# Performance work log

Measured on AMD Instinct MI355X. Metric: run time of the kernel, lower is better.

Reference implementation:

```python
import jax, jax.numpy as jnp
import numpy as np

N, H, MSG, OUT = 512, 128, 128, 64
F1, F2 = 256, 256  # f_dims (also used for g_mlp per source)
GOUT = 128         # hardcoded output_gmlp_dim
O1 = 256           # o_dims


def _p(key, shape, scale):
    return jax.random.normal(key, shape, dtype=jnp.float32) * scale


def setup_inputs() -> dict:
    key = jax.random.key(0)
    ks = jax.random.split(key, 24)
    s = lambda fan_in: 1.0 / np.sqrt(fan_in)
    inp = {
        "x": jax.random.normal(ks[0], (N, H), dtype=jnp.float32),
        "hidden": jax.random.normal(ks[1], (N, H), dtype=jnp.float32),
        "h0": jnp.zeros((1, N, H), dtype=jnp.float32),
        "c0": jnp.zeros((1, N, H), dtype=jnp.float32),
        # f MLP: 2H -> F1 -> F2 -> MSG
        "Wf1": _p(ks[2], (F1, 2 * H), s(2 * H)), "bf1": jnp.zeros((F1,), jnp.float32),
        "Wf2": _p(ks[3], (F2, F1), s(F1)), "bf2": jnp.zeros((F2,), jnp.float32),
        "Wf3": _p(ks[4], (MSG, F2), s(F2)), "bf3": jnp.zeros((MSG,), jnp.float32),
        # g_mlp: H+MSG -> F1 -> F2 -> GOUT
        "Wg1": _p(ks[5], (F1, H + MSG), s(H + MSG)), "bg1": jnp.zeros((F1,), jnp.float32),
        "Wg2": _p(ks[6], (F2, F1), s(F1)), "bg2": jnp.zeros((F2,), jnp.float32),
        "Wg3": _p(ks[7], (GOUT, F2), s(F2)), "bg3": jnp.zeros((GOUT,), jnp.float32),
        # LSTM (1 layer): GOUT -> H, gate order i,f,g,o
        "W_ih": _p(ks[8], (4 * H, GOUT), s(H)), "W_hh": _p(ks[9], (4 * H, H), s(H)),
        "b_ih": jnp.zeros((4 * H,), jnp.float32), "b_hh": jnp.zeros((4 * H,), jnp.float32),
        # o MLP: H -> O1 -> OUT
        "Wo1": _p(ks[10], (O1, H), s(H)), "bo1": jnp.zeros((O1,), jnp.float32),
        "Wo2": _p(ks[11], (OUT, O1), s(O1)), "bo2": jnp.zeros((OUT,), jnp.float32),
    }
    return inp


def reference(x, hidden, h0, c0,
              Wf1, bf1, Wf2, bf2, Wf3, bf3,
              Wg1, bg1, Wg2, bg2, Wg3, bg3,
              W_ih, W_hh, b_ih, b_hh,
              Wo1, bo1, Wo2, bo2):
    # --- pairwise message MLP f(cat(hidden[i], hidden[j])) over all (i,j) ---
    # split first-layer weight to avoid materializing [N,N,2H] concat
    A = hidden @ Wf1[:, :H].T            # [N, F1], contribution of node i
    B = hidden @ Wf1[:, H:].T            # [N, F1], contribution of node j
    h1 = jax.nn.relu(A[:, None, :] + B[None, :, :] + bf1)   # [N, N, F1]
    h2 = jax.nn.relu(h1 @ Wf2.T + bf2)                       # [N, N, F2]
    messages = h2 @ Wf3.T + bf3                              # [N, N, MSG]
    sum_messages = jnp.sum(messages, axis=0)                 # [N, MSG] (sum over i)

    # --- g_mlp on cat(x, sum_messages) ---
    g_in = jnp.concatenate([x, sum_messages], axis=1)        # [N, H+MSG]
    g1 = jax.nn.relu(g_in @ Wg1.T + bg1)
    g2 = jax.nn.relu(g1 @ Wg2.T + bg2)
    input_g = g2 @ Wg3.T + bg3                               # [N, GOUT]

    # --- single-step LSTM (seq_len=1, batch=N), PyTorch gate order i,f,g,o ---
    gates = input_g @ W_ih.T + b_ih + h0[0] @ W_hh.T + b_hh  # [N, 4H]
    i_g, f_g, g_g, o_g = jnp.split(gates, 4, axis=1)
    i_g = jax.nn.sigmoid(i_g); f_g = jax.nn.sigmoid(f_g)
    g_g = jnp.tanh(g_g); o_g = jax.nn.sigmoid(o_g)
    c_new = f_g * c0[0] + i_g * g_g
    hidden_new = o_g * jnp.tanh(c_new)                       # [N, H]

    # --- output MLP o (single_output=False) ---
    o1 = jax.nn.relu(hidden_new @ Wo1.T + bo1)
    out = o1 @ Wo2.T + bo2                                   # [N, OUT]

    return (out, hidden_new, hidden_new[None], c_new[None])
```

## Files before the change

### kernel.cpp

```cpp
#include <hip/hip_runtime.h>
#include <hip/hip_bf16.h>


#define NN   512
#define HH   128
#define F1D  256
#define F2D  256
#define OUTD 64
#define ICHUNK 64

typedef _Float16 half_t;
typedef _Float16 half8 __attribute__((ext_vector_type(8)));
typedef float float4_t __attribute__((ext_vector_type(4)));
typedef float float8_t __attribute__((ext_vector_type(8)));

__device__ __forceinline__ float sigmoidf_(float x) {
    return 1.0f / (1.0f + __expf(-x));
}

#define HL_INV 2.44140625e-4f

#define WS_TAIL_B 1835008
#define WS_WT1_B  3342336
#define T3H 0
#define G1H 65536
#define G2H 196608
#define G3H 327680
#define CATH 393216
#define O1H 655360
#define O2H 720896

__constant__ int p_cum[8]   = {16, 24, 40, 56, 64, 96, 112, 116};
__constant__ int p_K[8]     = {256, 256, 256, 256, 256, 256, 128, 256};
__constant__ int p_hioff[8] = {0, T3H, G1H, G2H, G3H, CATH, O1H, O2H};
__constant__ int p_cnt[8]   = {65536, 32768, 65536, 65536, 32768, 131072, 32768, 16384};

__global__ __launch_bounds__(256)
void k0_prep(const float* __restrict__ Wf1,
             const float* __restrict__ Wf2,
             const float* __restrict__ Wf3,
             const float* __restrict__ Wg1, const float* __restrict__ Wg2,
             const float* __restrict__ Wg3,
             const float* __restrict__ W_ih, const float* __restrict__ W_hh,
             const float* __restrict__ Wo1, const float* __restrict__ Wo2,
             half_t* __restrict__ tail,
             half_t* __restrict__ W2H, half_t* __restrict__ W2L,
             float* __restrict__ WT1) {
    __shared__ float slab[4096];
    __shared__ float tile[64][65];
    const int t = threadIdx.x;
    const int bid = blockIdx.x;

    if (bid < 116) {
        int m = 0;
        while (m < 7 && bid >= p_cum[m]) ++m;
        const int pl = bid - (m ? p_cum[m - 1] : 0);
        const int K = p_K[m];
        const int kshift = (K == 256) ? 8 : 7;
        const int n0 = pl * 16;

        const float* src;
        switch (m) {
            case 0: src = Wf2; break;
            case 1: src = Wf3; break;
            case 2: src = Wg1; break;
            case 3: src = Wg2; break;
            case 4: src = Wg3; break;
            case 6: src = Wo1; break;
            default: src = Wo2; break;
        }
        for (int q = t; q < (16 * K) / 4; q += 256) {
            const int flat = q * 4;
            const int r = flat >> kshift;
            const int k = flat & (K - 1);
            float4_t v;
            if (m == 5) {
                v = (k < 128) ? *(const float4_t*)(W_ih + (n0 + r) * 128 + k)
                              : *(const float4_t*)(W_hh + (n0 + r) * 128 + (k - 128));
            } else {
                v = *(const float4_t*)(src + (size_t)(n0 + r) * K + k);
            }
            *(float4_t*)&slab[flat] = v;
        }
        __syncthreads();

        half_t *hi, *lo;
        if (m == 0) { hi = W2H; lo = W2L; }
        else        { hi = tail + p_hioff[m]; lo = hi + p_cnt[m]; }
        const int base = pl * (K << 4);
        for (int f0 = t * 8; f0 < 16 * K; f0 += 2048) {
            const int ks = f0 >> 9;
            const int g4 = (f0 >> 7) & 3;
            const int l15 = (f0 >> 3) & 15;
            const int k0 = ks * 32 + g4 * 8;
            float8_t v = *(const float8_t*)&slab[l15 * K + k0];
            half8 hv, lv;
#pragma unroll
            for (int e = 0; e < 8; ++e) {
                half_t h = (half_t)v[e];
                hv[e] = h;
                lv[e] = (half_t)((v[e] - (float)h) * 4096.0f);
            }
            *(half8*)(hi + base + f0) = hv;
            *(half8*)(lo + base + f0) = lv;
        }
    } else {
        const int local = bid - 116;
        const int tr = local >> 2, tc = local & 3;
#pragma unroll
        for (int q = 0; q < 16; ++q) {
            const int idx = q * 256 + t;
            const int ly = idx >> 6, lx = idx & 63;
            tile[ly][lx] = Wf1[(tr * 64 + ly) * 256 + tc * 64 + lx];
        }
        __syncthreads();
#pragma unroll
        for (int q = 0; q < 16; ++q) {
            const int idx = q * 256 + t;
            const int ly = idx >> 6, lx = idx & 63;
            WT1[(tc * 64 + ly) * 256 + tr * 64 + lx] = tile[lx][ly];
        }
    }
}

__global__ __launch_bounds__(256)
void k1_proj(const float* __restrict__ hidden,
             const float* __restrict__ WT1,
             const float* __restrict__ bf1,
             float* __restrict__ A32,
             float* __restrict__ B32) {
    __shared__ float hid[4][HH];
    const int t = threadIdx.x;
    const int i0 = blockIdx.x * 4;
    for (int q = t; q < 4 * HH; q += 256)
        hid[q >> 7][q & 127] = hidden[(i0 + (q >> 7)) * HH + (q & 127)];
    __syncthreads();

    float accA[4], accB[4];
    const float b = bf1[t];
#pragma unroll
    for (int r = 0; r < 4; ++r) { accA[r] = b; accB[r] = 0.0f; }

    const float* wcol = WT1 + t;
#pragma unroll 4
    for (int kk = 0; kk < HH; ++kk) {
        const float va = wcol[kk * 256];
        const float vb = wcol[(kk + 128) * 256];
#pragma unroll
        for (int r = 0; r < 4; ++r) {
            const float h = hid[r][kk];
            accA[r] = fmaf(h, va, accA[r]);
            accB[r] = fmaf(h, vb, accB[r]);
        }
    }
#pragma unroll
    for (int r = 0; r < 4; ++r) {
        A32[(i0 + r) * F1D + t] = accA[r];
        B32[(i0 + r) * F1D + t] = accB[r];
    }
}

__global__ __launch_bounds__(512, 2)
void k2_pairwise(const float* __restrict__ A32,
                 const float* __restrict__ B32,
                 const half_t* __restrict__ W2H,
                 const half_t* __restrict__ W2L,
                 const float* __restrict__ bf2,
                 float* __restrict__ S) {
    __shared__ half_t hbuf[2][8][512];

    const int tid = threadIdx.x;
    const int lane = tid & 63;
    const int w = tid >> 6;
    const int l15 = lane & 15;
    const int g4 = lane >> 4;
    const int j0 = blockIdx.y * 16;
    const int i0 = blockIdx.x * ICHUNK;

    const half8* WH8 = (const half8*)W2H;
    const half8* WL8 = (const half8*)W2L;
    half8 Wh[2][8], Wl[2][8];
#pragma unroll
    for (int nt = 0; nt < 2; ++nt)
#pragma unroll
        for (int ks = 0; ks < 8; ++ks) {
            const int idx = (w * 2 + nt) * 512 + ks * 64 + lane;
            Wh[nt][ks] = WH8[idx];
            Wl[nt][ks] = WL8[idx];
        }
#pragma unroll
    for (int nt = 0; nt < 2; ++nt)
#pragma unroll
        for (int ks = 0; ks < 8; ++ks) {
            asm volatile("" : "+v"(Wh[nt][ks]));
            asm volatile("" : "+v"(Wl[nt][ks]));
        }

    float4_t Bw0 = *(const float4_t*)(B32 + (size_t)(j0 + l15) * F1D + w * 32 + g4 * 8);
    float4_t Bw1 = *(const float4_t*)(B32 + (size_t)(j0 + l15) * F1D + w * 32 + g4 * 8 + 4);
    asm volatile("" : "+v"(Bw0));
    asm volatile("" : "+v"(Bw1));

    float b2v[2];
#pragma unroll
    for (int nt = 0; nt < 2; ++nt) b2v[nt] = bf2[w * 32 + nt * 16 + l15];

    float4_t acc[2];
#pragma unroll
    for (int nt = 0; nt < 2; ++nt)
#pragma unroll
        for (int r = 0; r < 4; ++r) acc[nt][r] = 0.0f;

    {
        const float* Ap = A32 + (size_t)i0 * F1D + w * 32 + g4 * 8;
        float4_t a0 = *(const float4_t*)Ap;
        float4_t a1 = *(const float4_t*)(Ap + 4);
        half8 hf;
#pragma unroll
        for (int e = 0; e < 4; ++e) {
            hf[e]     = (half_t)fmaxf(a0[e] + Bw0[e], 0.0f);
            hf[4 + e] = (half_t)fmaxf(a1[e] + Bw1[e], 0.0f);
        }
        *(half8*)&hbuf[0][w][lane * 8] = hf;
    }
    __syncthreads();

    int p = 0;
    for (int io = 0; io < ICHUNK; ++io) {
        float4_t a0, a1;
        if (io + 1 < ICHUNK) {
            const float* Ap = A32 + (size_t)(i0 + io + 1) * F1D + w * 32 + g4 * 8;
            a0 = *(const float4_t*)Ap;
            a1 = *(const float4_t*)(Ap + 4);
        }

        float4_t C[2], Cl[2];
#pragma unroll
        for (int nt = 0; nt < 2; ++nt)
#pragma unroll
            for (int r = 0; r < 4; ++r) { C[nt][r] = 0.0f; Cl[nt][r] = 0.0f; }

#pragma unroll
        for (int ks = 0; ks < 8; ++ks) {
            half8 hf = *(const half8*)&hbuf[p][ks][lane * 8];
            C[0]  = __builtin_amdgcn_mfma_f32_16x16x32_f16(hf, Wh[0][ks], C[0], 0, 0, 0);
            C[1]  = __builtin_amdgcn_mfma_f32_16x16x32_f16(hf, Wh[1][ks], C[1], 0, 0, 0);
            Cl[0] = __builtin_amdgcn_mfma_f32_16x16x32_f16(hf, Wl[0][ks], Cl[0], 0, 0, 0);
            Cl[1] = __builtin_amdgcn_mfma_f32_16x16x32_f16(hf, Wl[1][ks], Cl[1], 0, 0, 0);
        }

        if (io + 1 < ICHUNK) {
            half8 hf;
#pragma unroll
            for (int e = 0; e < 4; ++e) {
                hf[e]     = (half_t)fmaxf(a0[e] + Bw0[e], 0.0f);
                hf[4 + e] = (half_t)fmaxf(a1[e] + Bw1[e], 0.0f);
            }
            *(half8*)&hbuf[p ^ 1][w][lane * 8] = hf;
        }

#pragma unroll
        for (int nt = 0; nt < 2; ++nt) {
#pragma unroll
            for (int r = 0; r < 4; ++r) {
                float v = fmaf(Cl[nt][r], HL_INV, C[nt][r]) + b2v[nt];
                acc[nt][r] += fmaxf(v, 0.0f);
            }
        }
        __syncthreads();
        p ^= 1;
    }

#pragma unroll
    for (int nt = 0; nt < 2; ++nt)
#pragma unroll
        for (int r = 0; r < 4; ++r)
            atomicAdd(&S[(size_t)(j0 + g4 * 4 + r) * F2D + w * 32 + nt * 16 + l15], acc[nt][r]);
}

#define AST 260

template<int NT, int NKS>
__device__ __forceinline__ void frag_gemm(const float* __restrict__ aPtr,
                                          const half_t* __restrict__ WhF,
                                          const half_t* __restrict__ WlF,
                                          const int* pB, int lane8,
                                          float4_t* Chi, float4_t* Clo) {
#pragma unroll
    for (int ks = 0; ks < NKS; ++ks) {
        float4_t a0 = *(const float4_t*)(aPtr + ks * 32);
        float4_t a1 = *(const float4_t*)(aPtr + ks * 32 + 4);
        half8 ah, al;
#pragma unroll
        for (int e = 0; e < 4; ++e) {
            half_t h0 = (half_t)a0[e];
            ah[e] = h0; al[e] = (half_t)((a0[e] - (float)h0) * 4096.0f);
            half_t h1 = (half_t)a1[e];
            ah[4+e] = h1; al[4+e] = (half_t)((a1[e] - (float)h1) * 4096.0f);
        }
#pragma unroll
        for (int nt = 0; nt < NT; ++nt) {
            half8 wh = *(const half8*)(WhF + pB[nt] + ks * 512 + lane8);
            half8 wl = *(const half8*)(WlF + pB[nt] + ks * 512 + lane8);
            Chi[nt] = __builtin_amdgcn_mfma_f32_16x16x32_f16(ah, wh, Chi[nt], 0, 0, 0);
            Clo[nt] = __builtin_amdgcn_mfma_f32_16x16x32_f16(ah, wl, Clo[nt], 0, 0, 0);
            Clo[nt] = __builtin_amdgcn_mfma_f32_16x16x32_f16(al, wh, Clo[nt], 0, 0, 0);
        }
    }
}

__global__ __launch_bounds__(512)
void k4_tail(const float* __restrict__ S,
             const float* __restrict__ x,
             const float* __restrict__ h0,
             const float* __restrict__ c0,
             const half_t* __restrict__ tail,
             const float* __restrict__ bf3,
             const float* __restrict__ bg1, const float* __restrict__ bg2,
             const float* __restrict__ bg3,
             const float* __restrict__ b_ih, const float* __restrict__ b_hh,
             const float* __restrict__ bo1, const float* __restrict__ bo2,
             float* __restrict__ out,
             float* __restrict__ hid_out,
             float* __restrict__ h_out,
             float* __restrict__ c_out) {
    __shared__ float bufA[16 * AST];
    __shared__ float bufB[16 * AST];
    __shared__ float bufC[16 * AST];
    const int tid = threadIdx.x;
    const int lane = tid & 63;
    const int w = tid >> 6;
    const int l15 = lane & 15;
    const int g4 = lane >> 4;
    const int r0 = blockIdx.x * 16;
    const int lane8 = lane * 8;

    for (int q = tid; q < 16 * 256; q += 512)
        bufC[(q >> 8) * AST + (q & 255)] = S[(size_t)(r0 + (q >> 8)) * 256 + (q & 255)];
    for (int q = tid; q < 16 * 128; q += 512)
        bufA[(q >> 7) * AST + (q & 127)] = x[(r0 + (q >> 7)) * 128 + (q & 127)];
    __syncthreads();

    const float* aFrag;
    int pB[4];
    float4_t Chi[4], Clo[4];

    {
        const int n = w * 16 + l15;
        pB[0] = w * 4096;
        Chi[0] = float4_t{0,0,0,0}; Clo[0] = float4_t{0,0,0,0};
        aFrag = bufC + l15 * AST + g4 * 8;
        frag_gemm<1, 8>(aFrag, tail + T3H, tail + T3H + 32768, pB, lane8, Chi, Clo);
        const float b = 512.0f * bf3[n];
#pragma unroll
        for (int r = 0; r < 4; ++r)
            bufA[(g4 * 4 + r) * AST + 128 + n] = Chi[0][r] + Clo[0][r] * HL_INV + b;
    }
    __syncthreads();

    {
        pB[0] = (w * 2) * 4096; pB[1] = (w * 2 + 1) * 4096;
        Chi[0] = float4_t{0,0,0,0}; Clo[0] = float4_t{0,0,0,0};
        Chi[1] = float4_t{0,0,0,0}; Clo[1] = float4_t{0,0,0,0};
        aFrag = bufA + l15 * AST + g4 * 8;
        frag_gemm<2, 8>(aFrag, tail + G1H, tail + G1H + 65536, pB, lane8, Chi, Clo);
#pragma unroll
        for (int nt = 0; nt < 2; ++nt) {
            const int n = w * 32 + nt * 16 + l15;
            const float b = bg1[n];
#pragma unroll
            for (int r = 0; r < 4; ++r)
                bufB[(g4 * 4 + r) * AST + n] = fmaxf(Chi[nt][r] + Clo[nt][r] * HL_INV + b, 0.0f);
        }
    }
    __syncthreads();

    {
        pB[0] = (w * 2) * 4096; pB[1] = (w * 2 + 1) * 4096;
        Chi[0] = float4_t{0,0,0,0}; Clo[0] = float4_t{0,0,0,0};
        Chi[1] = float4_t{0,0,0,0}; Clo[1] = float4_t{0,0,0,0};
        aFrag = bufB + l15 * AST + g4 * 8;
        frag_gemm<2, 8>(aFrag, tail + G2H, tail + G2H + 65536, pB, lane8, Chi, Clo);
#pragma unroll
        for (int nt = 0; nt < 2; ++nt) {
            const int n = w * 32 + nt * 16 + l15;
            const float b = bg2[n];
#pragma unroll
            for (int r = 0; r < 4; ++r)
                bufC[(g4 * 4 + r) * AST + n] = fmaxf(Chi[nt][r] + Clo[nt][r] * HL_INV + b, 0.0f);
        }
        for (int q = tid; q < 16 * 128; q += 512)
            bufA[(q >> 7) * AST + 128 + (q & 127)] = h0[(r0 + (q >> 7)) * 128 + (q & 127)];
    }
    __syncthreads();

    {
        const int n = w * 16 + l15;
        pB[0] = w * 4096;
        Chi[0] = float4_t{0,0,0,0}; Clo[0] = float4_t{0,0,0,0};
        aFrag = bufC + l15 * AST + g4 * 8;
        frag_gemm<1, 8>(aFrag, tail + G3H, tail + G3H + 32768, pB, lane8, Chi, Clo);
        const float b = bg3[n];
#pragma unroll
        for (int r = 0; r < 4; ++r)
            bufA[(g4 * 4 + r) * AST + n] = Chi[0][r] + Clo[0][r] * HL_INV + b;
    }
    __syncthreads();

    {
#pragma unroll
        for (int nt = 0; nt < 4; ++nt) {
            pB[nt] = (w + nt * 8) * 4096;
            Chi[nt] = float4_t{0,0,0,0}; Clo[nt] = float4_t{0,0,0,0};
        }
        aFrag = bufA + l15 * AST + g4 * 8;
        frag_gemm<4, 8>(aFrag, tail + CATH, tail + CATH + 131072, pB, lane8, Chi, Clo);

        const int nh = w * 16 + l15;
        float bi = b_ih[nh]       + b_hh[nh];
        float bf = b_ih[128 + nh] + b_hh[128 + nh];
        float bg = b_ih[256 + nh] + b_hh[256 + nh];
        float bo = b_ih[384 + nh] + b_hh[384 + nh];
#pragma unroll
        for (int r = 0; r < 4; ++r) {
            const int row = r0 + g4 * 4 + r;
            float gi = sigmoidf_(Chi[0][r] + Clo[0][r] * HL_INV + bi);
            float gf = sigmoidf_(Chi[1][r] + Clo[1][r] * HL_INV + bf);
            float gg = tanhf(    Chi[2][r] + Clo[2][r] * HL_INV + bg);
            float go = sigmoidf_(Chi[3][r] + Clo[3][r] * HL_INV + bo);
            float c = gf * c0[row * 128 + nh] + gi * gg;
            float h = go * tanhf(c);
            bufC[(g4 * 4 + r) * AST + nh] = h;
            hid_out[row * 128 + nh] = h;
            h_out[row * 128 + nh]   = h;
            c_out[row * 128 + nh]   = c;
        }
    }
    __syncthreads();

    {
        pB[0] = (w * 2) * 2048; pB[1] = (w * 2 + 1) * 2048;
        Chi[0] = float4_t{0,0,0,0}; Clo[0] = float4_t{0,0,0,0};
        Chi[1] = float4_t{0,0,0,0}; Clo[1] = float4_t{0,0,0,0};
        aFrag = bufC + l15 * AST + g4 * 8;
        frag_gemm<2, 4>(aFrag, tail + O1H, tail + O1H + 32768, pB, lane8, Chi, Clo);
#pragma unroll
        for (int nt = 0; nt < 2; ++nt) {
            const int n = w * 32 + nt * 16 + l15;
            const float b = bo1[n];
#pragma unroll
            for (int r = 0; r < 4; ++r)
                bufB[(g4 * 4 + r) * AST + n] = fmaxf(Chi[nt][r] + Clo[nt][r] * HL_INV + b, 0.0f);
        }
    }
    __syncthreads();

    if (w < 4) {
        const int n = w * 16 + l15;
        pB[0] = w * 4096;
        Chi[0] = float4_t{0,0,0,0}; Clo[0] = float4_t{0,0,0,0};
        aFrag = bufB + l15 * AST + g4 * 8;
        frag_gemm<1, 8>(aFrag, tail + O2H, tail + O2H + 16384, pB, lane8, Chi, Clo);
        const float b = bo2[n];
#pragma unroll
        for (int r = 0; r < 4; ++r)
            out[(r0 + g4 * 4 + r) * OUTD + n] = Chi[0][r] + Clo[0][r] * HL_INV + b;
    }
}

extern "C" void kernel_launch(void* const* d_in, const int* in_sizes, int n_in,
                              void* d_out, int out_size, void* d_ws, size_t ws_size,
                              hipStream_t stream) {
    const float* x      = (const float*)d_in[0];
    const float* hidden = (const float*)d_in[1];
    const float* h0     = (const float*)d_in[2];
    const float* c0     = (const float*)d_in[3];
    const float* Wf1    = (const float*)d_in[4];
    const float* bf1    = (const float*)d_in[5];
    const float* Wf2    = (const float*)d_in[6];
    const float* bf2    = (const float*)d_in[7];
    const float* Wf3    = (const float*)d_in[8];
    const float* bf3    = (const float*)d_in[9];
    const float* Wg1    = (const float*)d_in[10];
    const float* bg1    = (const float*)d_in[11];
    const float* Wg2    = (const float*)d_in[12];
    const float* bg2    = (const float*)d_in[13];
    const float* Wg3    = (const float*)d_in[14];
    const float* bg3    = (const float*)d_in[15];
    const float* W_ih   = (const float*)d_in[16];
    const float* W_hh   = (const float*)d_in[17];
    const float* b_ih   = (const float*)d_in[18];
    const float* b_hh   = (const float*)d_in[19];
    const float* Wo1    = (const float*)d_in[20];
    const float* bo1    = (const float*)d_in[21];
    const float* Wo2    = (const float*)d_in[22];
    const float* bo2    = (const float*)d_in[23];

    char* wsb = (char*)d_ws;
    float*  A32  = (float*)(wsb + 0);
    float*  B32  = (float*)(wsb + 524288);
    half_t* W2H  = (half_t*)(wsb + 1048576);
    half_t* W2L  = (half_t*)(wsb + 1179648);
    float*  S    = (float*)(wsb + 1310720);
    half_t* tail = (half_t*)(wsb + WS_TAIL_B);
    float*  WT1  = (float*)(wsb + WS_WT1_B);

    float* outp  = (float*)d_out;
    float* hid1  = (float*)d_out + 32768;
    float* hid2  = (float*)d_out + 98304;
    float* cout  = (float*)d_out + 163840;

    hipMemsetAsync(S, 0, (size_t)NN * F2D * sizeof(float), stream);

    k0_prep<<<dim3(132), dim3(256), 0, stream>>>(Wf1, Wf2, Wf3, Wg1, Wg2, Wg3,
                                                 W_ih, W_hh, Wo1, Wo2,
                                                 tail, W2H, W2L, WT1);

    k1_proj<<<dim3(128), dim3(256), 0, stream>>>(hidden, WT1, bf1, A32, B32);

    k2_pairwise<<<dim3(8, 32), dim3(512), 0, stream>>>(A32, B32, W2H, W2L, bf2, S);

    k4_tail<<<dim3(32), dim3(512), 0, stream>>>(S, x, h0, c0, tail,
                                                bf3, bg1, bg2, bg3,
                                                b_ih, b_hh, bo1, bo2,
                                                outp, hid1, hid2, cout);
}
```

Baseline: 213.6 us.

## Batch eight i-rows per barrier in pairwise kernel with double-buffered LDS

Restructures the pairwise k2 loop so each LDS stage holds eight i-rows instead of one. This cuts __syncthreads from 64 to 8 per block, and prefetches the next chunk's A rows in two halves so they overlap the MFMA work. LDS use rises from 16KB to 128KB per block, which limits how many blocks fit per CU (launch bounds ask for 2). It also raises register pressure from holding the prefetched rows.

Result: slower. 423.3 us (+98.2%).

```diff
diff --git a/kernel.cpp b/kernel.cpp
--- a/kernel.cpp
+++ b/kernel.cpp
@@ -167,7 +167,7 @@
                  const half_t* __restrict__ W2L,
                  const float* __restrict__ bf2,
                  float* __restrict__ S) {
-    __shared__ half_t hbuf[2][8][512];
+    __shared__ half_t hbuf[2][8][8][512];
 
     const int tid = threadIdx.x;
     const int lane = tid & 63;
@@ -176,6 +176,7 @@
     const int g4 = lane >> 4;
     const int j0 = blockIdx.y * 16;
     const int i0 = blockIdx.x * ICHUNK;
+    const int lane8 = lane * 8;
 
     const half8* WH8 = (const half8*)W2H;
     const half8* WL8 = (const half8*)W2L;
@@ -198,8 +199,6 @@
 
     float4_t Bw0 = *(const float4_t*)(B32 + (size_t)(j0 + l15) * F1D + w * 32 + g4 * 8);
     float4_t Bw1 = *(const float4_t*)(B32 + (size_t)(j0 + l15) * F1D + w * 32 + g4 * 8 + 4);
-    asm volatile("" : "+v"(Bw0));
-    asm volatile("" : "+v"(Bw1));
 
     float b2v[2];
 #pragma unroll
@@ -211,8 +210,9 @@
 #pragma unroll
         for (int r = 0; r < 4; ++r) acc[nt][r] = 0.0f;
 
-    {
-        const float* Ap = A32 + (size_t)i0 * F1D + w * 32 + g4 * 8;
+#pragma unroll
+    for (int q = 0; q < 8; ++q) {
+        const float* Ap = A32 + (size_t)(i0 + q) * F1D + w * 32 + g4 * 8;
         float4_t a0 = *(const float4_t*)Ap;
         float4_t a1 = *(const float4_t*)(Ap + 4);
         half8 hf;
@@ -221,54 +221,105 @@
             hf[e]     = (half_t)fmaxf(a0[e] + Bw0[e], 0.0f);
             hf[4 + e] = (half_t)fmaxf(a1[e] + Bw1[e], 0.0f);
         }
-        *(half8*)&hbuf[0][w][lane * 8] = hf;
-    }
-    __syncthreads();
-
-    int p = 0;
-    for (int io = 0; io < ICHUNK; ++io) {
-        float4_t a0, a1;
-        if (io + 1 < ICHUNK) {
-            const float* Ap = A32 + (size_t)(i0 + io + 1) * F1D + w * 32 + g4 * 8;
-            a0 = *(const float4_t*)Ap;
-            a1 = *(const float4_t*)(Ap + 4);
-        }
-
-        float4_t C[2], Cl[2];
-#pragma unroll
-        for (int nt = 0; nt < 2; ++nt)
-#pragma unroll
-            for (int r = 0; r < 4; ++r) { C[nt][r] = 0.0f; Cl[nt][r] = 0.0f; }
-
-#pragma unroll
-        for (int ks = 0; ks < 8; ++ks) {
-            half8 hf = *(const half8*)&hbuf[p][ks][lane * 8];
-            C[0]  = __builtin_amdgcn_mfma_f32_16x16x32_f16(hf, Wh[0][ks], C[0], 0, 0, 0);
-            C[1]  = __builtin_amdgcn_mfma_f32_16x16x32_f16(hf, Wh[1][ks], C[1], 0, 0, 0);
-            Cl[0] = __builtin_amdgcn_mfma_f32_16x16x32_f16(hf, Wl[0][ks], Cl[0], 0, 0, 0);
-            Cl[1] = __builtin_amdgcn_mfma_f32_16x16x32_f16(hf, Wl[1][ks], Cl[1], 0, 0, 0);
-        }
-
-        if (io + 1 < ICHUNK) {
-            half8 hf;
-#pragma unroll
-            for (int e = 0; e < 4; ++e) {
-                hf[e]     = (half_t)fmaxf(a0[e] + Bw0[e], 0.0f);
-                hf[4 + e] = (half_t)fmaxf(a1[e] + Bw1[e], 0.0f);
-            }
-            *(half8*)&hbuf[p ^ 1][w][lane * 8] = hf;
-        }
-
-#pragma unroll
-        for (int nt = 0; nt < 2; ++nt) {
-#pragma unroll
-            for (int r = 0; r < 4; ++r) {
-                float v = fmaf(Cl[nt][r], HL_INV, C[nt][r]) + b2v[nt];
-                acc[nt][r] += fmaxf(v, 0.0f);
+        *(half8*)&hbuf[0][q][w][lane8] = hf;
+    }
+    __syncthreads();
+
+    for (int c = 0; c < 8; ++c) {
+        const int cur = c & 1;
+        const int nxt = cur ^ 1;
+        const int inext = i0 + (c + 1) * 8;
+
+        float4_t av[4][2];
+        if (c < 7) {
+#pragma unroll
+            for (int q = 0; q < 4; ++q) {
+                const float* Ap = A32 + (size_t)(inext + q) * F1D + w * 32 + g4 * 8;
+                av[q][0] = *(const float4_t*)Ap;
+                av[q][1] = *(const float4_t*)(Ap + 4);
+            }
+        }
+
+#pragma unroll
+        for (int q = 0; q < 4; ++q) {
+            float4_t C[2], Cl[2];
+#pragma unroll
+            for (int nt = 0; nt < 2; ++nt)
+#pragma unroll
+                for (int r = 0; r < 4; ++r) { C[nt][r] = 0.0f; Cl[nt][r] = 0.0f; }
+#pragma unroll
+            for (int ks = 0; ks < 8; ++ks) {
+                half8 hf = *(const half8*)&hbuf[cur][q][ks][lane8];
+                C[0]  = __builtin_amdgcn_mfma_f32_16x16x32_f16(hf, Wh[0][ks], C[0], 0, 0, 0);
+                C[1]  = __builtin_amdgcn_mfma_f32_16x16x32_f16(hf, Wh[1][ks], C[1], 0, 0, 0);
+                Cl[0] = __builtin_amdgcn_mfma_f32_16x16x32_f16(hf, Wl[0][ks], Cl[0], 0, 0, 0);
+                Cl[1] = __builtin_amdgcn_mfma_f32_16x16x32_f16(hf, Wl[1][ks], Cl[1], 0, 0, 0);
+            }
+#pragma unroll
+            for (int nt = 0; nt < 2; ++nt)
+#pragma unroll
+                for (int r = 0; r < 4; ++r) {
+                    float v = fmaf(Cl[nt][r], HL_INV, C[nt][r]) + b2v[nt];
+                    acc[nt][r] += fmaxf(v, 0.0f);
+                }
+        }
+
+        if (c < 7) {
+#pragma unroll
+            for (int q = 0; q < 4; ++q) {
+                half8 hf;
+#pragma unroll
+                for (int e = 0; e < 4; ++e) {
+                    hf[e]     = (half_t)fmaxf(av[q][0][e] + Bw0[e], 0.0f);
+                    hf[4 + e] = (half_t)fmaxf(av[q][1][e] + Bw1[e], 0.0f);
+                }
+                *(half8*)&hbuf[nxt][q][w][lane8] = hf;
+            }
+#pragma unroll
+            for (int q = 0; q < 4; ++q) {
+                const float* Ap = A32 + (size_t)(inext + 4 + q) * F1D + w * 32 + g4 * 8;
+                av[q][0] = *(const float4_t*)Ap;
+                av[q][1] = *(const float4_t*)(Ap + 4);
+            }
+        }
+
+#pragma unroll
+        for (int q = 4; q < 8; ++q) {
+            float4_t C[2], Cl[2];
+#pragma unroll
+            for (int nt = 0; nt < 2; ++nt)
+#pragma unroll
+                for (int r = 0; r < 4; ++r) { C[nt][r] = 0.0f; Cl[nt][r] = 0.0f; }
+#pragma unroll
+            for (int ks = 0; ks < 8; ++ks) {
+                half8 hf = *(const half8*)&hbuf[cur][q][ks][lane8];
+                C[0]  = __builtin_amdgcn_mfma_f32_16x16x32_f16(hf, Wh[0][ks], C[0], 0, 0, 0);
+                C[1]  = __builtin_amdgcn_mfma_f32_16x16x32_f16(hf, Wh[1][ks], C[1], 0, 0, 0);
+                Cl[0] = __builtin_amdgcn_mfma_f32_16x16x32_f16(hf, Wl[0][ks], Cl[0], 0, 0, 0);
+                Cl[1] = __builtin_amdgcn_mfma_f32_16x16x32_f16(hf, Wl[1][ks], Cl[1], 0, 0, 0);
+            }
+#pragma unroll
+            for (int nt = 0; nt < 2; ++nt)
+#pragma unroll
+                for (int r = 0; r < 4; ++r) {
+                    float v = fmaf(Cl[nt][r], HL_INV, C[nt][r]) + b2v[nt];
+                    acc[nt][r] += fmaxf(v, 0.0f);
+                }
+        }
+
+        if (c < 7) {
+#pragma unroll
+            for (int q = 0; q < 4; ++q) {
+                half8 hf;
+#pragma unroll
+                for (int e = 0; e < 4; ++e) {
+                    hf[e]     = (half_t)fmaxf(av[q][0][e] + Bw0[e], 0.0f);
+                    hf[4 + e] = (half_t)fmaxf(av[q][1][e] + Bw1[e], 0.0f);
+                }
+                *(half8*)&hbuf[nxt][4 + q][w][lane8] = hf;
             }
         }
         __syncthreads();
-        p ^= 1;
     }
 
 #pragma unroll
```
